# Performance work log

Hardware: AMD Instinct MI355X
Metric: run time of the kernel (lower is better)

Reference implementation:

```python
import jax, jax.numpy as jnp
import numpy as np

QMIN, QMAX = 0.0, 255.0  # uint8 activation quantization range


def _qlinear(x, w_q, b, s_in, zp_in, s_w):
    """zentorch_qlinear: quantize fp32 x to uint8, int8 weight, dequant output.

    x:   [M, K] fp32
    w_q: [N, K] int8 values (stored int32), symmetric (weight zp = 0)
    b:   [N] fp32
    s_in, zp_in: scalars (activation scale / zero point)
    s_w: [N] per-output-channel weight scales
    """
    zp = zp_in.astype(jnp.float32)
    q = jnp.clip(jnp.round(x / s_in) + zp, QMIN, QMAX)      # fake-quant uint8
    x_dq = (q - zp) * s_in                                   # dequantized activation
    w_dq = w_q.astype(jnp.float32) * s_w[:, None]            # [N, K] dequant weight
    return x_dq @ w_dq.T + b                                 # [M, N] fp32


def setup_inputs() -> dict:
    key = jax.random.key(0)
    k1, k2, k3, k4 = jax.random.split(key, 4)
    M, K, N = 8192, 4096, 4096
    inp = {
        "input": jax.random.normal(k1, (M, K), dtype=jnp.float32),
        "weights": jax.random.randint(k2, (N, K), -128, 128, dtype=jnp.int32),
        "biases": jax.random.normal(k3, (N,), dtype=jnp.float32) * 0.1,
        "input_scales": jnp.array([0.05], dtype=jnp.float32),
        "input_zero_points": jnp.array([128], dtype=jnp.int32),
        "weight_scales": jax.random.uniform(k4, (N,), dtype=jnp.float32, minval=0.001, maxval=0.01),
        "weight_zero_points": jnp.zeros((N,), dtype=jnp.int32),
        "output_dtype": 0,  # 0 -> float32
    }
    return inp


def reference(input, weights, biases, input_scales, input_zero_points,
              weight_scales, weight_zero_points, output_dtype):
    s_in = input_scales[0]
    zp_in = input_zero_points[0]
    x = _qlinear(input, weights, biases, s_in, zp_in, weight_scales)
    x = _qlinear(x, weights, biases, s_in, zp_in, weight_scales)
    x = _qlinear(x, weights, biases, s_in, zp_in, weight_scales)
    return x
```

## Files before the change

kernel.cpp:

```cpp
#include <hip/hip_runtime.h>
#include <stdint.h>

#define M_DIM 8192
#define K_DIM 4096
#define N_DIM 4096
#define KTILES (K_DIM / 64)

typedef __attribute__((ext_vector_type(4))) int i32x4;

__global__ void pack_w_kernel(const int* __restrict__ w, char* __restrict__ wp,
                              int* __restrict__ corr, const int* __restrict__ zpp) {
  __shared__ int red[256];
  const int n = blockIdx.x;
  const int t = threadIdx.x;
  const int4* row = (const int4*)(w + (size_t)n * K_DIM);
  int s = 0;
  int words[4];
#pragma unroll
  for (int u = 0; u < 4; ++u) {
    int4 v = row[t * 4 + u];
    s += v.x + v.y + v.z + v.w;
    words[u] = (v.x & 255) | ((v.y & 255) << 8) | ((v.z & 255) << 16) | (v.w << 24);
  }
  ((int4*)(wp + (size_t)n * K_DIM))[t] = make_int4(words[0], words[1], words[2], words[3]);
  red[t] = s;
  __syncthreads();
  for (int off = 128; off > 0; off >>= 1) {
    if (t < off) red[t] += red[t + off];
    __syncthreads();
  }
  if (t == 0) corr[n] = (128 - zpp[0]) * red[0];
}

__global__ void quant_in_kernel(const float* __restrict__ x, char* __restrict__ q,
                                const float* __restrict__ sp, const int* __restrict__ zpp) {
  const int i = blockIdx.x * blockDim.x + threadIdx.x;
  const float s = sp[0];
  const float zp = (float)zpp[0];
  float4 v = ((const float4*)x)[i];
  float t0 = fminf(fmaxf(rintf(v.x / s) + zp, 0.f), 255.f);
  float t1 = fminf(fmaxf(rintf(v.y / s) + zp, 0.f), 255.f);
  float t2 = fminf(fmaxf(rintf(v.z / s) + zp, 0.f), 255.f);
  float t3 = fminf(fmaxf(rintf(v.w / s) + zp, 0.f), 255.f);
  int b0 = (int)t0 - 128, b1 = (int)t1 - 128, b2 = (int)t2 - 128, b3 = (int)t3 - 128;
  ((int*)q)[i] = (b0 & 255) | ((b1 & 255) << 8) | ((b2 & 255) << 16) | (b3 << 24);
}

#define STAGE16(SRC, DST)                                                     \
  __builtin_amdgcn_global_load_lds(                                           \
      (const __attribute__((address_space(1))) void*)(SRC),                   \
      (__attribute__((address_space(3))) void*)(DST), 16, 0, 0)

#define RD(p) (*(const i32x4*)(p))

#define TILE(SLOT, KSTG, DO_NEXT)                                             \
  {                                                                           \
    const char* bufA_ = &lds[SLOT][0][0];                                     \
    char* nA_ = &lds[((SLOT) + 3) & 3][0][0];                                 \
    char* nB_ = &lds[((SLOT) + 3) & 3][1][0];                                 \
    i32x4 a1_[4];                                                             \
    _Pragma("unroll") for (int i_ = 0; i_ < 4; ++i_)                          \
        a1_[i_] = RD(bufA_ + aoff[4 + i_]);                                   \
    STAGE16(asrc0 + (size_t)(KSTG) * 64, nA_ + o0_);                          \
    STAGE16(asrc1 + (size_t)(KSTG) * 64, nA_ + o1_);                          \
    __builtin_amdgcn_s_setprio(1);                                            \
    _Pragma("unroll") for (int i_ = 0; i_ < 4; ++i_)                          \
        _Pragma("unroll") for (int j_ = 0; j_ < 4; ++j_)                      \
            acc[i_][j_] = __builtin_amdgcn_mfma_i32_16x16x64_i8(              \
                a0[i_], b0[j_], acc[i_][j_], 0, 0, 0);                        \
    __builtin_amdgcn_s_setprio(0);                                            \
    i32x4 ta_[4], tb_[4];                                                     \
    if (DO_NEXT) {                                                            \
      const char* xA_ = &lds[((SLOT) + 1) & 3][0][0];                         \
      const char* xB_ = &lds[((SLOT) + 1) & 3][1][0];                         \
      _Pragma("unroll") for (int i_ = 0; i_ < 4; ++i_)                        \
          ta_[i_] = RD(xA_ + aoff[i_]);                                       \
      _Pragma("unroll") for (int j_ = 0; j_ < 4; ++j_)                        \
          tb_[j_] = RD(xB_ + boff[j_]);                                       \
    }                                                                         \
    STAGE16(bsrc0 + (size_t)(KSTG) * 64, nB_ + o0_);                          \
    STAGE16(bsrc1 + (size_t)(KSTG) * 64, nB_ + o1_);                          \
    __builtin_amdgcn_s_setprio(1);                                            \
    _Pragma("unroll") for (int i_ = 0; i_ < 4; ++i_)                          \
        _Pragma("unroll") for (int j_ = 0; j_ < 4; ++j_)                      \
            acc[4 + i_][j_] = __builtin_amdgcn_mfma_i32_16x16x64_i8(          \
                a1_[i_], b0[j_], acc[4 + i_][j_], 0, 0, 0);                   \
    __builtin_amdgcn_s_setprio(0);                                            \
    asm volatile("s_waitcnt vmcnt(4)" ::: "memory");                          \
    __builtin_amdgcn_s_barrier();                                             \
    if (DO_NEXT) {                                                            \
      _Pragma("unroll") for (int i_ = 0; i_ < 4; ++i_) a0[i_] = ta_[i_];      \
      _Pragma("unroll") for (int j_ = 0; j_ < 4; ++j_) b0[j_] = tb_[j_];      \
    }                                                                         \
  }

template <int WRITE_Q>
__global__ __launch_bounds__(512, 2) void gemm_kernel(
    const char* __restrict__ qa, const char* __restrict__ wb,
    const int* __restrict__ corr, const float* __restrict__ swp,
    const float* __restrict__ bias, const float* __restrict__ sp,
    const int* __restrict__ zpp, char* __restrict__ outq, float* __restrict__ outf) {
  __shared__ __align__(16) char lds[4][2][16384];
  const int tid = threadIdx.x;
  const int lane = tid & 63;
  const int w = tid >> 6;
  const int wr = w >> 2;
  const int wc = w & 3;
  const int bid = blockIdx.x;
  const int bm = bid & 31;
  const int bn = bid >> 5;
  const char* abase = qa + (size_t)bm * 256 * K_DIM;
  const char* bbase = wb + (size_t)bn * 256 * K_DIM;

  const int o0_ = tid * 16;
  const int o1_ = 8192 + tid * 16;
  const int r0_ = o0_ >> 6, r1_ = o1_ >> 6;
  const int g0_ = ((o0_ >> 4) & 3) ^ ((r0_ >> 1) & 3);
  const int g1_ = ((o1_ >> 4) & 3) ^ ((r1_ >> 1) & 3);
  const char* asrc0 = abase + (size_t)r0_ * K_DIM + g0_ * 16;
  const char* asrc1 = abase + (size_t)r1_ * K_DIM + g1_ * 16;
  const int p0_ = (r0_ & ~63) + 4 * (r0_ & 15) + ((r0_ >> 4) & 3);
  const int p1_ = (r1_ & ~63) + 4 * (r1_ & 15) + ((r1_ >> 4) & 3);
  const char* bsrc0 = bbase + (size_t)p0_ * K_DIM + g0_ * 16;
  const char* bsrc1 = bbase + (size_t)p1_ * K_DIM + g1_ * 16;

  const int rr = lane & 15;
  const int g = lane >> 4;
  int aoff[8], boff[4];
#pragma unroll
  for (int i = 0; i < 8; ++i) {
    const int row = wr * 128 + i * 16 + rr;
    aoff[i] = (row << 6) + ((g ^ ((row >> 1) & 3)) << 4);
  }
#pragma unroll
  for (int j = 0; j < 4; ++j) {
    const int row = wc * 64 + j * 16 + rr;
    boff[j] = (row << 6) + ((g ^ ((row >> 1) & 3)) << 4);
  }

  i32x4 acc[8][4] = {};

  STAGE16(asrc0, &lds[0][0][o0_]); STAGE16(asrc1, &lds[0][0][o1_]);
  STAGE16(bsrc0, &lds[0][1][o0_]); STAGE16(bsrc1, &lds[0][1][o1_]);
  STAGE16(asrc0 + 64, &lds[1][0][o0_]); STAGE16(asrc1 + 64, &lds[1][0][o1_]);
  STAGE16(bsrc0 + 64, &lds[1][1][o0_]); STAGE16(bsrc1 + 64, &lds[1][1][o1_]);
  STAGE16(asrc0 + 128, &lds[2][0][o0_]); STAGE16(asrc1 + 128, &lds[2][0][o1_]);
  STAGE16(bsrc0 + 128, &lds[2][1][o0_]); STAGE16(bsrc1 + 128, &lds[2][1][o1_]);
  asm volatile("s_waitcnt vmcnt(4)" ::: "memory");
  __builtin_amdgcn_s_barrier();

  i32x4 a0[4], b0[4];
#pragma unroll
  for (int i = 0; i < 4; ++i) a0[i] = RD(&lds[0][0][0] + aoff[i]);
#pragma unroll
  for (int j = 0; j < 4; ++j) b0[j] = RD(&lds[0][1][0] + boff[j]);

  for (int tb = 0; tb < (KTILES - 4) / 4; ++tb) {
    const int t0 = tb * 4;
#pragma unroll
    for (int u = 0; u < 4; ++u) {
      TILE(u, t0 + u + 3, 1);
    }
  }
  TILE(0, KTILES - 1, 1);
  TILE(1, KTILES - 1, 1);
  TILE(2, KTILES - 1, 1);
  TILE(3, KTILES - 1, 0);
  asm volatile("s_waitcnt vmcnt(0)" ::: "memory");

  const float s = sp[0];
  const float zpf = (float)zpp[0];
  const int m0 = bm * 256 + wr * 128 + (lane >> 4) * 4;
  const int nb4 = bn * 256 + wc * 64 + ((lane & 15) << 2);
  const int4 cr4 = *(const int4*)(corr + nb4);
  const float4 sw4 = *(const float4*)(swp + nb4);
  const float4 bb4 = *(const float4*)(bias + nb4);
  const float fs0 = s * sw4.x, fs1 = s * sw4.y, fs2 = s * sw4.z, fs3 = s * sw4.w;
#pragma unroll
  for (int i = 0; i < 8; ++i) {
#pragma unroll
    for (int q = 0; q < 4; ++q) {
      const int m = m0 + i * 16 + q;
      const float v0 = fs0 * (float)(acc[i][0][q] + cr4.x) + bb4.x;
      const float v1 = fs1 * (float)(acc[i][1][q] + cr4.y) + bb4.y;
      const float v2 = fs2 * (float)(acc[i][2][q] + cr4.z) + bb4.z;
      const float v3 = fs3 * (float)(acc[i][3][q] + cr4.w) + bb4.w;
      if (WRITE_Q) {
        const int b0i = (int)fminf(fmaxf(rintf(v0 / s) + zpf, 0.f), 255.f) - 128;
        const int b1i = (int)fminf(fmaxf(rintf(v1 / s) + zpf, 0.f), 255.f) - 128;
        const int b2i = (int)fminf(fmaxf(rintf(v2 / s) + zpf, 0.f), 255.f) - 128;
        const int b3i = (int)fminf(fmaxf(rintf(v3 / s) + zpf, 0.f), 255.f) - 128;
        const uint32_t pk = (uint32_t)(b0i & 255) | ((uint32_t)(b1i & 255) << 8) |
                            ((uint32_t)(b2i & 255) << 16) | ((uint32_t)b3i << 24);
        *(uint32_t*)(outq + (size_t)m * N_DIM + nb4) = pk;
      } else {
        float4 o4;
        o4.x = v0; o4.y = v1; o4.z = v2; o4.w = v3;
        *(float4*)(outf + (size_t)m * N_DIM + nb4) = o4;
      }
    }
  }
}

extern "C" void kernel_launch(void* const* d_in, const int* in_sizes, int n_in,
                              void* d_out, int out_size, void* d_ws, size_t ws_size,
                              hipStream_t stream) {
  const float* x = (const float*)d_in[0];
  const int* wq = (const int*)d_in[1];
  const float* bias = (const float*)d_in[2];
  const float* s_in = (const float*)d_in[3];
  const int* zp_in = (const int*)d_in[4];
  const float* s_w = (const float*)d_in[5];
  float* out = (float*)d_out;

  const size_t WP_BYTES = (size_t)N_DIM * K_DIM;
  const size_t Q_BYTES = (size_t)M_DIM * K_DIM;
  char* ws = (char*)d_ws;
  char* wp = ws;
  char* q1 = ws + WP_BYTES;
  char* q2 = q1 + Q_BYTES;
  int* corr = (int*)(q2 + Q_BYTES);
  const size_t NEEDED = WP_BYTES + 2 * Q_BYTES + (size_t)N_DIM * sizeof(int);
  if (ws_size < NEEDED) return;

  pack_w_kernel<<<N_DIM, 256, 0, stream>>>(wq, wp, corr, zp_in);
  quant_in_kernel<<<(M_DIM * K_DIM / 4) / 256, 256, 0, stream>>>(x, q1, s_in, zp_in);

  dim3 grid((M_DIM / 256) * (N_DIM / 256));
  dim3 blk(512);
  gemm_kernel<1><<<grid, blk, 0, stream>>>(q1, wp, corr, s_w, bias, s_in, zp_in, q2, nullptr);
  gemm_kernel<1><<<grid, blk, 0, stream>>>(q2, wp, corr, s_w, bias, s_in, zp_in, q1, nullptr);
  gemm_kernel<0><<<grid, blk, 0, stream>>>(q1, wp, corr, s_w, bias, s_in, zp_in, nullptr, out);
}
```

Before: 440.8 us.

## Pre-pack weights in MFMA fragment order and load B directly to registers

The weight packing kernel now writes int8 weights in a per-fragment layout, so each lane's 16-byte B operand for a 16-row group and k-tile sits contiguously. The GEMM then skips LDS staging for B and reads B fragments straight from global memory into registers one tile ahead. This halves LDS use and removes the B LDS reads and writes. The cost is that B loads now go through the vector memory path with no cross-wave sharing, which relies on the cache for reuse, and the vmcnt waits are adjusted to match.

```diff
diff --git a/kernel.cpp b/kernel.cpp
--- a/kernel.cpp
+++ b/kernel.cpp
@@ -13,16 +13,24 @@
   __shared__ int red[256];
   const int n = blockIdx.x;
   const int t = threadIdx.x;
-  const int4* row = (const int4*)(w + (size_t)n * K_DIM);
+  const int kt = t >> 2;
+  const int g = t & 3;
+  const int* row = w + (size_t)n * K_DIM + kt * 64 + g * 16;
   int s = 0;
   int words[4];
 #pragma unroll
   for (int u = 0; u < 4; ++u) {
-    int4 v = row[t * 4 + u];
+    int4 v = *(const int4*)(row + u * 4);
     s += v.x + v.y + v.z + v.w;
     words[u] = (v.x & 255) | ((v.y & 255) << 8) | ((v.z & 255) << 16) | (v.w << 24);
   }
-  ((int4*)(wp + (size_t)n * K_DIM))[t] = make_int4(words[0], words[1], words[2], words[3]);
+  const int b = n & ~63;
+  const int idx = n & 63;
+  const int j = idx & 3;
+  const int r = idx >> 2;
+  const int F = (b >> 4) + j;
+  char* dst = wp + ((size_t)F * 64 + kt) * 1024 + (g * 16 + r) * 16;
+  *(int4*)dst = make_int4(words[0], words[1], words[2], words[3]);
   red[t] = s;
   __syncthreads();
   for (int off = 128; off > 0; off >>= 1) {
@@ -53,11 +61,10 @@
 
 #define RD(p) (*(const i32x4*)(p))
 
-#define TILE(SLOT, KSTG, DO_NEXT)                                             \
+#define TILE(SLOT, KSTG, TN, DO_NEXT)                                         \
   {                                                                           \
-    const char* bufA_ = &lds[SLOT][0][0];                                     \
-    char* nA_ = &lds[((SLOT) + 3) & 3][0][0];                                 \
-    char* nB_ = &lds[((SLOT) + 3) & 3][1][0];                                 \
+    const char* bufA_ = &lds[SLOT][0];                                        \
+    char* nA_ = &lds[((SLOT) + 3) & 3][0];                                    \
     i32x4 a1_[4];                                                             \
     _Pragma("unroll") for (int i_ = 0; i_ < 4; ++i_)                          \
         a1_[i_] = RD(bufA_ + aoff[4 + i_]);                                   \
@@ -69,38 +76,35 @@
             acc[i_][j_] = __builtin_amdgcn_mfma_i32_16x16x64_i8(              \
                 a0[i_], b0[j_], acc[i_][j_], 0, 0, 0);                        \
     __builtin_amdgcn_s_setprio(0);                                            \
-    i32x4 ta_[4], tb_[4];                                                     \
+    i32x4 ta_[4], bn_[4];                                                     \
     if (DO_NEXT) {                                                            \
-      const char* xA_ = &lds[((SLOT) + 1) & 3][0][0];                         \
-      const char* xB_ = &lds[((SLOT) + 1) & 3][1][0];                         \
+      const char* xA_ = &lds[((SLOT) + 1) & 3][0];                            \
       _Pragma("unroll") for (int i_ = 0; i_ < 4; ++i_)                        \
           ta_[i_] = RD(xA_ + aoff[i_]);                                       \
       _Pragma("unroll") for (int j_ = 0; j_ < 4; ++j_)                        \
-          tb_[j_] = RD(xB_ + boff[j_]);                                       \
+          bn_[j_] = RD(bptr[j_] + (size_t)(TN) * 1024);                       \
     }                                                                         \
-    STAGE16(bsrc0 + (size_t)(KSTG) * 64, nB_ + o0_);                          \
-    STAGE16(bsrc1 + (size_t)(KSTG) * 64, nB_ + o1_);                          \
     __builtin_amdgcn_s_setprio(1);                                            \
     _Pragma("unroll") for (int i_ = 0; i_ < 4; ++i_)                          \
         _Pragma("unroll") for (int j_ = 0; j_ < 4; ++j_)                      \
             acc[4 + i_][j_] = __builtin_amdgcn_mfma_i32_16x16x64_i8(          \
                 a1_[i_], b0[j_], acc[4 + i_][j_], 0, 0, 0);                   \
     __builtin_amdgcn_s_setprio(0);                                            \
-    asm volatile("s_waitcnt vmcnt(4)" ::: "memory");                          \
+    asm volatile("s_waitcnt vmcnt(12)" ::: "memory");                         \
     __builtin_amdgcn_s_barrier();                                             \
     if (DO_NEXT) {                                                            \
       _Pragma("unroll") for (int i_ = 0; i_ < 4; ++i_) a0[i_] = ta_[i_];      \
-      _Pragma("unroll") for (int j_ = 0; j_ < 4; ++j_) b0[j_] = tb_[j_];      \
+      _Pragma("unroll") for (int j_ = 0; j_ < 4; ++j_) b0[j_] = bn_[j_];      \
     }                                                                         \
   }
 
 template <int WRITE_Q>
 __global__ __launch_bounds__(512, 2) void gemm_kernel(
-    const char* __restrict__ qa, const char* __restrict__ wb,
+    const char* __restrict__ qa, const char* __restrict__ wbp,
     const int* __restrict__ corr, const float* __restrict__ swp,
     const float* __restrict__ bias, const float* __restrict__ sp,
     const int* __restrict__ zpp, char* __restrict__ outq, float* __restrict__ outf) {
-  __shared__ __align__(16) char lds[4][2][16384];
+  __shared__ __align__(16) char lds[4][16384];
   const int tid = threadIdx.x;
   const int lane = tid & 63;
   const int w = tid >> 6;
@@ -110,7 +114,6 @@
   const int bm = bid & 31;
   const int bn = bid >> 5;
   const char* abase = qa + (size_t)bm * 256 * K_DIM;
-  const char* bbase = wb + (size_t)bn * 256 * K_DIM;
 
   const int o0_ = tid * 16;
   const int o1_ = 8192 + tid * 16;
@@ -119,53 +122,46 @@
   const int g1_ = ((o1_ >> 4) & 3) ^ ((r1_ >> 1) & 3);
   const char* asrc0 = abase + (size_t)r0_ * K_DIM + g0_ * 16;
   const char* asrc1 = abase + (size_t)r1_ * K_DIM + g1_ * 16;
-  const int p0_ = (r0_ & ~63) + 4 * (r0_ & 15) + ((r0_ >> 4) & 3);
-  const int p1_ = (r1_ & ~63) + 4 * (r1_ & 15) + ((r1_ >> 4) & 3);
-  const char* bsrc0 = bbase + (size_t)p0_ * K_DIM + g0_ * 16;
-  const char* bsrc1 = bbase + (size_t)p1_ * K_DIM + g1_ * 16;
+
+  const int Fbase = (bn * 256 + wc * 64) >> 4;
+  const char* bptr[4];
+#pragma unroll
+  for (int j = 0; j < 4; ++j)
+    bptr[j] = wbp + (size_t)(Fbase + j) * 64 * 1024 + lane * 16;
 
   const int rr = lane & 15;
   const int g = lane >> 4;
-  int aoff[8], boff[4];
+  int aoff[8];
 #pragma unroll
   for (int i = 0; i < 8; ++i) {
     const int row = wr * 128 + i * 16 + rr;
     aoff[i] = (row << 6) + ((g ^ ((row >> 1) & 3)) << 4);
   }
-#pragma unroll
-  for (int j = 0; j < 4; ++j) {
-    const int row = wc * 64 + j * 16 + rr;
-    boff[j] = (row << 6) + ((g ^ ((row >> 1) & 3)) << 4);
-  }
 
   i32x4 acc[8][4] = {};
 
-  STAGE16(asrc0, &lds[0][0][o0_]); STAGE16(asrc1, &lds[0][0][o1_]);
-  STAGE16(bsrc0, &lds[0][1][o0_]); STAGE16(bsrc1, &lds[0][1][o1_]);
-  STAGE16(asrc0 + 64, &lds[1][0][o0_]); STAGE16(asrc1 + 64, &lds[1][0][o1_]);
-  STAGE16(bsrc0 + 64, &lds[1][1][o0_]); STAGE16(bsrc1 + 64, &lds[1][1][o1_]);
-  STAGE16(asrc0 + 128, &lds[2][0][o0_]); STAGE16(asrc1 + 128, &lds[2][0][o1_]);
-  STAGE16(bsrc0 + 128, &lds[2][1][o0_]); STAGE16(bsrc1 + 128, &lds[2][1][o1_]);
-  asm volatile("s_waitcnt vmcnt(4)" ::: "memory");
+  STAGE16(asrc0, &lds[0][o0_]); STAGE16(asrc1, &lds[0][o1_]);
+  STAGE16(asrc0 + 64, &lds[1][o0_]); STAGE16(asrc1 + 64, &lds[1][o1_]);
+  STAGE16(asrc0 + 128, &lds[2][o0_]); STAGE16(asrc1 + 128, &lds[2][o1_]);
+  i32x4 a0[4], b0[4];
+#pragma unroll
+  for (int j = 0; j < 4; ++j) b0[j] = RD(bptr[j]);
+  asm volatile("s_waitcnt vmcnt(8)" ::: "memory");
   __builtin_amdgcn_s_barrier();
-
-  i32x4 a0[4], b0[4];
-#pragma unroll
-  for (int i = 0; i < 4; ++i) a0[i] = RD(&lds[0][0][0] + aoff[i]);
-#pragma unroll
-  for (int j = 0; j < 4; ++j) b0[j] = RD(&lds[0][1][0] + boff[j]);
+#pragma unroll
+  for (int i = 0; i < 4; ++i) a0[i] = RD(&lds[0][0] + aoff[i]);
 
   for (int tb = 0; tb < (KTILES - 4) / 4; ++tb) {
     const int t0 = tb * 4;
 #pragma unroll
     for (int u = 0; u < 4; ++u) {
-      TILE(u, t0 + u + 3, 1);
+      TILE(u, t0 + u + 3, t0 + u + 1, 1);
     }
   }
-  TILE(0, KTILES - 1, 1);
-  TILE(1, KTILES - 1, 1);
-  TILE(2, KTILES - 1, 1);
-  TILE(3, KTILES - 1, 0);
+  TILE(0, KTILES - 1, 61, 1);
+  TILE(1, KTILES - 1, 62, 1);
+  TILE(2, KTILES - 1, 63, 1);
+  TILE(3, KTILES - 1, 63, 0);
   asm volatile("s_waitcnt vmcnt(0)" ::: "memory");
 
   const float s = sp[0];
```

Result: slower. 450.5 us (+2.2%).
